# Kernel tuning notes

Hardware: AMD Instinct MI355X
Metric: run time of the kernel (lower is better)

Reference implementation:

```python
import jax, jax.numpy as jnp
import numpy as np

BATCH = 8192
N = 32
A_NUM = 5
EPS = 1e-10
ALPHA = jnp.array([0.01, 0.25, 0.5, 0.9, 0.99], dtype=jnp.float32)


def setup_inputs() -> dict:
    key = jax.random.key(0)
    ks = jax.random.split(key, 9)
    stdv = 1.0 / np.sqrt(N)
    u = lambda k, shape: jax.random.uniform(k, shape, jnp.float32, -stdv, stdv)
    L = N * (N - 1) // 2
    return {
        "inputs": jax.random.normal(ks[0], (BATCH, N, N), jnp.float32),
        "state": jax.random.normal(ks[1], (BATCH, A_NUM * N * N), jnp.float32),
        "WR_root": u(ks[2], (A_NUM,)),
        "Wt_root": u(ks[3], (1,)),
        "Wphi_root": u(ks[4], (1,)),
        "Ws_root": u(ks[5], (A_NUM,)),
        "Br": u(ks[6], (L, 1)),
        "Bt": u(ks[7], (L, 1)),
        "By": u(ks[8], (L, 1)),
    }


def _skew(Bvec, n):
    # Replicates the torch loop: row 0 is zeros; row k (k>=1) gets B[k-1 : 2k-1]
    # in its first k columns (overlapping slices of the flat parameter vector).
    b = Bvec.reshape(-1)
    r = jnp.arange(n)[:, None]
    c = jnp.arange(n)[None, :]
    idx = jnp.clip(r - 1 + c, 0, b.shape[0] - 1)  # B[k-1+j] for entry (k, j)
    L = jnp.where(c < r, b[idx], jnp.zeros((), b.dtype))
    return L - L.T


def _cayley(S, n):
    # MatrixExp in the source: (I - S)^{-1} (I + S)
    I = jnp.eye(n, dtype=S.dtype)
    return jnp.linalg.solve(I - S, I + S)


def _translate(A, Bvec, n):
    # M @ A @ M.T with M the Cayley 'exp' of the skew matrix built from Bvec.
    M = _cayley(_skew(Bvec, n), n)
    return jnp.einsum('ij,bjk,lk->bil', M, A, M)


def _nus(W_root, A, eps):
    # Weighted average over the a_num axis with weights W_root^2 / (sum + eps).
    W = W_root * W_root
    return jnp.einsum('a,banm->bnm', W / (W.sum() + eps), A)


def reference(inputs, state, WR_root, Wt_root, Wphi_root, Ws_root, Br, Bt, By):
    Mt_1 = state.reshape(-1, A_NUM, N, N)                 # [B, a, n, n]
    X = inputs.reshape(BATCH, N, N)                       # [B, n, n]

    Yt = _nus(WR_root, Mt_1, EPS)                         # [B, n, n]
    Rt = _translate(Yt, Br, N)

    at = (Wt_root[0] ** 2) / ((Wt_root ** 2 + Wphi_root ** 2).sum() + EPS)
    Tt = (1.0 - at) * X + at * Rt                         # Frechet mean FM
    Phit = _translate(Tt, Bt, N)

    # Per-j Frechet means, vectorized over the a_num axis.
    a = ALPHA[None, :, None, None]
    Mt = (1.0 - a) * Mt_1 + a * Phit[:, None, :, :]       # [B, a, n, n]

    St = _nus(Ws_root, Mt, EPS)
    Ot = _translate(St, By, N)                            # [B, n, n]

    return Ot, Mt.reshape(-1, A_NUM, N, N)
```

## Files before the change

### kernel.cpp

```cpp
#include <hip/hip_runtime.h>

#define NB 8192
#define OT_ELEMS (NB * 1024)
#define EPSF 1e-10f

typedef __attribute__((ext_vector_type(4))) float f32x4;
typedef __attribute__((ext_vector_type(8))) short s16x8;

#define SBAR() __builtin_amdgcn_sched_barrier(0)
#define LGK()  do { SBAR(); asm volatile("s_waitcnt lgkmcnt(0)"); SBAR(); } while (0)

#define MFMA_B16(A, B, C) __builtin_amdgcn_mfma_f32_16x16x32_bf16((A), (B), (C), 0, 0, 0)

__global__ void cayley_kernel(const float* __restrict__ Br,
                              const float* __restrict__ Bt,
                              const float* __restrict__ By,
                              float* __restrict__ M_out) {
  __shared__ float A[32][33];
  __shared__ float R[32][33];
  const float* B = (blockIdx.x == 0) ? Br : (blockIdx.x == 1) ? Bt : By;
  const int t = threadIdx.x;
  const int i = t >> 5, j = t & 31;
  float Lij = (j < i) ? B[i - 1 + j] : 0.0f;
  float Lji = (i < j) ? B[j - 1 + i] : 0.0f;
  float S = Lij - Lji;
  float eye = (i == j) ? 1.0f : 0.0f;
  A[i][j] = eye - S;
  R[i][j] = eye + S;
  __syncthreads();
  for (int p = 0; p < 32; ++p) {
    float f = A[i][p] / A[p][p];
    __syncthreads();
    if (i != p) {
      A[i][j] -= f * A[p][j];
      R[i][j] -= f * R[p][j];
    }
    __syncthreads();
  }
  M_out[blockIdx.x * 1024 + i * 32 + j] = R[i][j] / A[i][i];
}

__global__ void combine_kernel(float* __restrict__ ws) {
  __shared__ float sMR[1024], sMT[1024];
  const int t = threadIdx.x;
  sMR[t] = ws[t];
  sMT[t] = ws[1024 + t];
  __syncthreads();
  const int i = t >> 5, j = t & 31;
  float s = 0.f;
#pragma unroll
  for (int k = 0; k < 32; ++k)
    s = fmaf(sMT[i * 32 + k], sMR[k * 32 + j], s);
  ws[3072 + i * 32 + j] = s;
}

__device__ __forceinline__ void cvt_hilo8(const f32x4 f0, const f32x4 f1, s16x8& hi, s16x8& lo) {
  float f[8];
#pragma unroll
  for (int e = 0; e < 4; ++e) { f[e] = f0[e]; f[4 + e] = f1[e]; }
#pragma unroll
  for (int e = 0; e < 8; ++e) {
    unsigned u = __float_as_uint(f[e]);
    hi[e] = (short)(u >> 16);
    float ah = __uint_as_float(u & 0xffff0000u);
    lo[e] = (short)(__float_as_uint(f[e] - ah) >> 16);
  }
}

__device__ __forceinline__ void read_frag_lds(const float* sb, int off, s16x8& hi, s16x8& lo) {
  f32x4 f0 = *(const f32x4*)(sb + off);
  f32x4 f1 = *(const f32x4*)(sb + off + 4);
  cvt_hilo8(f0, f1, hi, lo);
}

__global__ __launch_bounds__(64) void spdsru_main(
    const float* __restrict__ X, const float* __restrict__ state,
    const float* __restrict__ WR, const float* __restrict__ Wt,
    const float* __restrict__ Wphi, const float* __restrict__ Ws,
    const float* __restrict__ Mg, float* __restrict__ out) {
  __shared__ __align__(16) float sb0[1152];
  __shared__ __align__(16) float sb1[1152];
  __shared__ __align__(16) float sb2[1152];
  __shared__ __align__(16) float sb3[1152];
  const int lane = threadIdx.x;
  const int l15 = lane & 15, l4 = lane >> 4;
  const int i0 = (lane >> 3) << 2, j0 = (lane & 7) << 2;
  const int bid = blockIdx.x;
  const int batch = (bid & 7) * (NB >> 3) + (bid >> 3);

  s16x8 Mh[3][2], Ml[3][2];
  {
    const int srcoff[3] = {1024, 3072, 2048};
#pragma unroll
    for (int q = 0; q < 3; ++q)
#pragma unroll
      for (int s = 0; s < 2; ++s) {
        const float* p = Mg + srcoff[q] + (16 * s + l15) * 32 + 8 * l4;
        cvt_hilo8(*(const f32x4*)p, *(const f32x4*)(p + 4), Mh[q][s], Ml[q][s]);
      }
  }

  const float alpha[5] = {0.01f, 0.25f, 0.5f, 0.9f, 0.99f};
  float wr[5], va[5];
  float cP = 0.f;
  {
    float sR = 0.f, sS = 0.f, wq[5];
#pragma unroll
    for (int a = 0; a < 5; ++a) { float v = WR[a]; wr[a] = v * v; sR += v * v; }
#pragma unroll
    for (int a = 0; a < 5; ++a) { float v = Ws[a]; wq[a] = v * v; sS += v * v; }
    const float invR = 1.0f / (sR + EPSF), invS = 1.0f / (sS + EPSF);
#pragma unroll
    for (int a = 0; a < 5; ++a) {
      wr[a] *= invR;
      float w = wq[a] * invS;
      va[a] = w * (1.0f - alpha[a]);
      cP += w * alpha[a];
    }
  }
  const float wt2 = Wt[0] * Wt[0], wp2 = Wphi[0] * Wphi[0];
  const float at = wt2 / (wt2 + wp2 + EPSF);
  const float omat = 1.0f - at;

  const float* xp = X + (size_t)batch * 1024;
  f32x4 x[4];
#pragma unroll
  for (int r = 0; r < 4; ++r)
    x[r] = __builtin_nontemporal_load((const f32x4*)(xp + (i0 + r) * 32 + j0));

  const float* stp = state + (size_t)batch * 5120;
  f32x4 U[4], V[4];
#pragma unroll
  for (int r = 0; r < 4; ++r) { U[r] = f32x4{0.f, 0.f, 0.f, 0.f}; V[r] = U[r]; }
#pragma unroll
  for (int a = 0; a < 5; ++a)
#pragma unroll
    for (int r = 0; r < 4; ++r) {
      const f32x4 v = *(const f32x4*)(stp + a * 1024 + (i0 + r) * 32 + j0);
      U[r] += wr[a] * v;
      V[r] += va[a] * v;
    }

#pragma unroll
  for (int c = 0; c < 4; ++c) {
    f32x4 cx = {x[0][c], x[1][c], x[2][c], x[3][c]};
    f32x4 cu = {U[0][c], U[1][c], U[2][c], U[3][c]};
    *(f32x4*)(sb0 + (j0 + c) * 36 + i0) = cx;
    *(f32x4*)(sb1 + (j0 + c) * 36 + i0) = cu;
  }
  LGK();

  s16x8 BXh[2], BXl[2], BUh[2], BUl[2];
#pragma unroll
  for (int s = 0; s < 2; ++s) {
    read_frag_lds(sb0, (16 * s + l15) * 36 + 8 * l4, BXh[s], BXl[s]);
    read_frag_lds(sb1, (16 * s + l15) * 36 + 8 * l4, BUh[s], BUl[s]);
  }
  {
    f32x4 gX[2][2], gU[2][2];
#pragma unroll
    for (int ms = 0; ms < 2; ++ms)
#pragma unroll
      for (int ns = 0; ns < 2; ++ns) {
        f32x4 a0 = {0.f, 0.f, 0.f, 0.f};
        a0 = MFMA_B16(Ml[0][ms], BXh[ns], a0);
        a0 = MFMA_B16(Mh[0][ms], BXl[ns], a0);
        a0 = MFMA_B16(Mh[0][ms], BXh[ns], a0);
        gX[ms][ns] = a0;
        f32x4 a1 = {0.f, 0.f, 0.f, 0.f};
        a1 = MFMA_B16(Ml[1][ms], BUh[ns], a1);
        a1 = MFMA_B16(Mh[1][ms], BUl[ns], a1);
        a1 = MFMA_B16(Mh[1][ms], BUh[ns], a1);
        gU[ms][ns] = a1;
      }
#pragma unroll
    for (int ms = 0; ms < 2; ++ms)
#pragma unroll
      for (int ns = 0; ns < 2; ++ns)
#pragma unroll
        for (int r = 0; r < 4; ++r) {
          sb2[(16 * ms + 4 * l4 + r) * 36 + 16 * ns + l15] = gX[ms][ns][r];
          sb3[(16 * ms + 4 * l4 + r) * 36 + 16 * ns + l15] = gU[ms][ns][r];
        }
  }
  LGK();

  {
    s16x8 AXh[2], AXl[2], AUh[2], AUl[2];
#pragma unroll
    for (int s = 0; s < 2; ++s) {
      read_frag_lds(sb2, (16 * s + l15) * 36 + 8 * l4, AXh[s], AXl[s]);
      read_frag_lds(sb3, (16 * s + l15) * 36 + 8 * l4, AUh[s], AUl[s]);
    }
    f32x4 ph[2][2];
#pragma unroll
    for (int ms = 0; ms < 2; ++ms)
#pragma unroll
      for (int ns = 0; ns < 2; ++ns) {
        f32x4 a0 = {0.f, 0.f, 0.f, 0.f};
        a0 = MFMA_B16(AXl[ms], Mh[0][ns], a0);
        a0 = MFMA_B16(AXh[ms], Ml[0][ns], a0);
        a0 = MFMA_B16(AXh[ms], Mh[0][ns], a0);
        f32x4 a1 = {0.f, 0.f, 0.f, 0.f};
        a1 = MFMA_B16(AUl[ms], Mh[1][ns], a1);
        a1 = MFMA_B16(AUh[ms], Ml[1][ns], a1);
        a1 = MFMA_B16(AUh[ms], Mh[1][ns], a1);
        ph[ms][ns] = omat * a0 + at * a1;
      }
#pragma unroll
    for (int ms = 0; ms < 2; ++ms)
#pragma unroll
      for (int ns = 0; ns < 2; ++ns)
#pragma unroll
        for (int r = 0; r < 4; ++r)
          sb0[(16 * ms + 4 * l4 + r) * 36 + 16 * ns + l15] = ph[ms][ns][r];
  }
  LGK();

  f32x4 ph4[4];
#pragma unroll
  for (int r = 0; r < 4; ++r)
    ph4[r] = *(const f32x4*)(sb0 + (i0 + r) * 36 + j0);
  f32x4 st4[4];
#pragma unroll
  for (int r = 0; r < 4; ++r) st4[r] = V[r] + cP * ph4[r];
#pragma unroll
  for (int c = 0; c < 4; ++c) {
    f32x4 cs = {st4[0][c], st4[1][c], st4[2][c], st4[3][c]};
    *(f32x4*)(sb1 + (j0 + c) * 36 + i0) = cs;
  }
  f32x4 raw2[20];
#pragma unroll
  for (int a = 0; a < 5; ++a)
#pragma unroll
    for (int r = 0; r < 4; ++r)
      raw2[a * 4 + r] = *(const f32x4*)(stp + a * 1024 + (i0 + r) * 32 + j0);
  LGK();

  {
    s16x8 BSh[2], BSl[2];
#pragma unroll
    for (int s = 0; s < 2; ++s)
      read_frag_lds(sb1, (16 * s + l15) * 36 + 8 * l4, BSh[s], BSl[s]);
    f32x4 gS[2][2];
#pragma unroll
    for (int ms = 0; ms < 2; ++ms)
#pragma unroll
      for (int ns = 0; ns < 2; ++ns) {
        f32x4 acc = {0.f, 0.f, 0.f, 0.f};
        acc = MFMA_B16(Ml[2][ms], BSh[ns], acc);
        acc = MFMA_B16(Mh[2][ms], BSl[ns], acc);
        acc = MFMA_B16(Mh[2][ms], BSh[ns], acc);
        gS[ms][ns] = acc;
      }
    float* outMt = out + OT_ELEMS + (size_t)batch * 5120;
#pragma unroll
    for (int a = 0; a < 5; ++a) {
      const float al = alpha[a], om = 1.0f - al;
#pragma unroll
      for (int r = 0; r < 4; ++r) {
        f32x4 w = om * raw2[a * 4 + r] + al * ph4[r];
        __builtin_nontemporal_store(w, (f32x4*)(outMt + a * 1024 + (i0 + r) * 32 + j0));
      }
    }
#pragma unroll
    for (int ms = 0; ms < 2; ++ms)
#pragma unroll
      for (int ns = 0; ns < 2; ++ns)
#pragma unroll
        for (int r = 0; r < 4; ++r)
          sb2[(16 * ms + 4 * l4 + r) * 36 + 16 * ns + l15] = gS[ms][ns][r];
  }
  LGK();

  {
    s16x8 ASh[2], ASl[2];
#pragma unroll
    for (int s = 0; s < 2; ++s)
      read_frag_lds(sb2, (16 * s + l15) * 36 + 8 * l4, ASh[s], ASl[s]);
    f32x4 o[2][2];
#pragma unroll
    for (int ms = 0; ms < 2; ++ms)
#pragma unroll
      for (int ns = 0; ns < 2; ++ns) {
        f32x4 acc = {0.f, 0.f, 0.f, 0.f};
        acc = MFMA_B16(ASl[ms], Mh[2][ns], acc);
        acc = MFMA_B16(ASh[ms], Ml[2][ns], acc);
        acc = MFMA_B16(ASh[ms], Mh[2][ns], acc);
        o[ms][ns] = acc;
      }
#pragma unroll
    for (int ms = 0; ms < 2; ++ms)
#pragma unroll
      for (int ns = 0; ns < 2; ++ns)
#pragma unroll
        for (int r = 0; r < 4; ++r)
          sb3[(16 * ms + 4 * l4 + r) * 36 + 16 * ns + l15] = o[ms][ns][r];
  }
  LGK();

  float* outOt = out + (size_t)batch * 1024;
#pragma unroll
  for (int r = 0; r < 4; ++r) {
    f32x4 ov = *(const f32x4*)(sb3 + (i0 + r) * 36 + j0);
    __builtin_nontemporal_store(ov, (f32x4*)(outOt + (i0 + r) * 32 + j0));
  }
}

extern "C" void kernel_launch(void* const* d_in, const int* in_sizes, int n_in,
                              void* d_out, int out_size, void* d_ws, size_t ws_size,
                              hipStream_t stream) {
  const float* X     = (const float*)d_in[0];
  const float* state = (const float*)d_in[1];
  const float* WR    = (const float*)d_in[2];
  const float* Wt    = (const float*)d_in[3];
  const float* Wphi  = (const float*)d_in[4];
  const float* Ws    = (const float*)d_in[5];
  const float* Br    = (const float*)d_in[6];
  const float* Bt    = (const float*)d_in[7];
  const float* By    = (const float*)d_in[8];
  float* m_ws = (float*)d_ws;
  float* outp = (float*)d_out;

  cayley_kernel<<<3, 1024, 0, stream>>>(Br, Bt, By, m_ws);
  combine_kernel<<<1, 1024, 0, stream>>>(m_ws);
  spdsru_main<<<NB, 64, 0, stream>>>(X, state, WR, Wt, Wphi, Ws, m_ws, outp);
}
```

Baseline: 89.18 us.

## Split S=V+cP*Phi left-product across stages and store Ot directly from MFMA

```diff
diff --git a/kernel.cpp b/kernel.cpp
--- a/kernel.cpp
+++ b/kernel.cpp
@@ -11,6 +11,13 @@
 #define LGK()  do { SBAR(); asm volatile("s_waitcnt lgkmcnt(0)"); SBAR(); } while (0)
 
 #define MFMA_B16(A, B, C) __builtin_amdgcn_mfma_f32_16x16x32_bf16((A), (B), (C), 0, 0, 0)
+
+#define PROD3(ACC, AH, AL, BH, BL)             \
+  do {                                         \
+    ACC = MFMA_B16((AL), (BH), ACC);           \
+    ACC = MFMA_B16((AH), (BL), ACC);           \
+    ACC = MFMA_B16((AH), (BH), ACC);           \
+  } while (0)
 
 __global__ void cayley_kernel(const float* __restrict__ Br,
                               const float* __restrict__ Bt,
@@ -82,6 +89,7 @@
   __shared__ __align__(16) float sb1[1152];
   __shared__ __align__(16) float sb2[1152];
   __shared__ __align__(16) float sb3[1152];
+  __shared__ __align__(16) float sb4[1152];
   const int lane = threadIdx.x;
   const int l15 = lane & 15, l4 = lane >> 4;
   const int i0 = (lane >> 3) << 2, j0 = (lane & 7) << 2;
@@ -145,33 +153,36 @@
   for (int c = 0; c < 4; ++c) {
     f32x4 cx = {x[0][c], x[1][c], x[2][c], x[3][c]};
     f32x4 cu = {U[0][c], U[1][c], U[2][c], U[3][c]};
+    f32x4 cv = {V[0][c], V[1][c], V[2][c], V[3][c]};
     *(f32x4*)(sb0 + (j0 + c) * 36 + i0) = cx;
     *(f32x4*)(sb1 + (j0 + c) * 36 + i0) = cu;
+    *(f32x4*)(sb2 + (j0 + c) * 36 + i0) = cv;
   }
   LGK();
 
-  s16x8 BXh[2], BXl[2], BUh[2], BUl[2];
-#pragma unroll
-  for (int s = 0; s < 2; ++s) {
-    read_frag_lds(sb0, (16 * s + l15) * 36 + 8 * l4, BXh[s], BXl[s]);
-    read_frag_lds(sb1, (16 * s + l15) * 36 + 8 * l4, BUh[s], BUl[s]);
-  }
-  {
+  f32x4 gV[2][2];
+  {
+    s16x8 BXh[2], BXl[2], BUh[2], BUl[2], BVh[2], BVl[2];
+#pragma unroll
+    for (int s = 0; s < 2; ++s) {
+      read_frag_lds(sb0, (16 * s + l15) * 36 + 8 * l4, BXh[s], BXl[s]);
+      read_frag_lds(sb1, (16 * s + l15) * 36 + 8 * l4, BUh[s], BUl[s]);
+      read_frag_lds(sb2, (16 * s + l15) * 36 + 8 * l4, BVh[s], BVl[s]);
+    }
     f32x4 gX[2][2], gU[2][2];
 #pragma unroll
     for (int ms = 0; ms < 2; ++ms)
 #pragma unroll
       for (int ns = 0; ns < 2; ++ns) {
         f32x4 a0 = {0.f, 0.f, 0.f, 0.f};
-        a0 = MFMA_B16(Ml[0][ms], BXh[ns], a0);
-        a0 = MFMA_B16(Mh[0][ms], BXl[ns], a0);
-        a0 = MFMA_B16(Mh[0][ms], BXh[ns], a0);
+        PROD3(a0, Mh[0][ms], Ml[0][ms], BXh[ns], BXl[ns]);
         gX[ms][ns] = a0;
         f32x4 a1 = {0.f, 0.f, 0.f, 0.f};
-        a1 = MFMA_B16(Ml[1][ms], BUh[ns], a1);
-        a1 = MFMA_B16(Mh[1][ms], BUl[ns], a1);
-        a1 = MFMA_B16(Mh[1][ms], BUh[ns], a1);
+        PROD3(a1, Mh[1][ms], Ml[1][ms], BUh[ns], BUl[ns]);
         gU[ms][ns] = a1;
+        f32x4 a2 = {0.f, 0.f, 0.f, 0.f};
+        PROD3(a2, Mh[2][ms], Ml[2][ms], BVh[ns], BVl[ns]);
+        gV[ms][ns] = a2;
       }
 #pragma unroll
     for (int ms = 0; ms < 2; ++ms)
@@ -179,8 +190,8 @@
       for (int ns = 0; ns < 2; ++ns)
 #pragma unroll
         for (int r = 0; r < 4; ++r) {
-          sb2[(16 * ms + 4 * l4 + r) * 36 + 16 * ns + l15] = gX[ms][ns][r];
-          sb3[(16 * ms + 4 * l4 + r) * 36 + 16 * ns + l15] = gU[ms][ns][r];
+          sb3[(16 * ms + 4 * l4 + r) * 36 + 16 * ns + l15] = gX[ms][ns][r];
+          sb4[(16 * ms + 4 * l4 + r) * 36 + 16 * ns + l15] = gU[ms][ns][r];
         }
   }
   LGK();
@@ -189,8 +200,8 @@
     s16x8 AXh[2], AXl[2], AUh[2], AUl[2];
 #pragma unroll
     for (int s = 0; s < 2; ++s) {
-      read_frag_lds(sb2, (16 * s + l15) * 36 + 8 * l4, AXh[s], AXl[s]);
-      read_frag_lds(sb3, (16 * s + l15) * 36 + 8 * l4, AUh[s], AUl[s]);
+      read_frag_lds(sb3, (16 * s + l15) * 36 + 8 * l4, AXh[s], AXl[s]);
+      read_frag_lds(sb4, (16 * s + l15) * 36 + 8 * l4, AUh[s], AUl[s]);
     }
     f32x4 ph[2][2];
 #pragma unroll
@@ -198,60 +209,70 @@
 #pragma unroll
       for (int ns = 0; ns < 2; ++ns) {
         f32x4 a0 = {0.f, 0.f, 0.f, 0.f};
-        a0 = MFMA_B16(AXl[ms], Mh[0][ns], a0);
-        a0 = MFMA_B16(AXh[ms], Ml[0][ns], a0);
-        a0 = MFMA_B16(AXh[ms], Mh[0][ns], a0);
+        PROD3(a0, AXh[ms], AXl[ms], Mh[0][ns], Ml[0][ns]);
         f32x4 a1 = {0.f, 0.f, 0.f, 0.f};
-        a1 = MFMA_B16(AUl[ms], Mh[1][ns], a1);
-        a1 = MFMA_B16(AUh[ms], Ml[1][ns], a1);
-        a1 = MFMA_B16(AUh[ms], Mh[1][ns], a1);
+        PROD3(a1, AUh[ms], AUl[ms], Mh[1][ns], Ml[1][ns]);
         ph[ms][ns] = omat * a0 + at * a1;
       }
 #pragma unroll
     for (int ms = 0; ms < 2; ++ms)
 #pragma unroll
       for (int ns = 0; ns < 2; ++ns)
-#pragma unroll
-        for (int r = 0; r < 4; ++r)
-          sb0[(16 * ms + 4 * l4 + r) * 36 + 16 * ns + l15] = ph[ms][ns][r];
+        *(f32x4*)(sb0 + (16 * ns + l15) * 36 + 16 * ms + 4 * l4) = ph[ms][ns];
   }
   LGK();
 
-  f32x4 ph4[4];
-#pragma unroll
-  for (int r = 0; r < 4; ++r)
-    ph4[r] = *(const f32x4*)(sb0 + (i0 + r) * 36 + j0);
-  f32x4 st4[4];
-#pragma unroll
-  for (int r = 0; r < 4; ++r) st4[r] = V[r] + cP * ph4[r];
-#pragma unroll
-  for (int c = 0; c < 4; ++c) {
-    f32x4 cs = {st4[0][c], st4[1][c], st4[2][c], st4[3][c]};
-    *(f32x4*)(sb1 + (j0 + c) * 36 + i0) = cs;
-  }
   f32x4 raw2[20];
 #pragma unroll
   for (int a = 0; a < 5; ++a)
 #pragma unroll
     for (int r = 0; r < 4; ++r)
       raw2[a * 4 + r] = *(const f32x4*)(stp + a * 1024 + (i0 + r) * 32 + j0);
+  f32x4 ph4[4];
+  {
+    s16x8 Bph_h[2], Bph_l[2];
+#pragma unroll
+    for (int s = 0; s < 2; ++s)
+      read_frag_lds(sb0, (16 * s + l15) * 36 + 8 * l4, Bph_h[s], Bph_l[s]);
+    f32x4 pc[4];
+#pragma unroll
+    for (int c = 0; c < 4; ++c)
+      pc[c] = *(const f32x4*)(sb0 + (j0 + c) * 36 + i0);
+#pragma unroll
+    for (int r = 0; r < 4; ++r)
+      ph4[r] = f32x4{pc[0][r], pc[1][r], pc[2][r], pc[3][r]};
+    f32x4 gS[2][2];
+#pragma unroll
+    for (int ms = 0; ms < 2; ++ms)
+#pragma unroll
+      for (int ns = 0; ns < 2; ++ns) {
+        f32x4 a2 = {0.f, 0.f, 0.f, 0.f};
+        PROD3(a2, Mh[2][ms], Ml[2][ms], Bph_h[ns], Bph_l[ns]);
+        gS[ms][ns] = gV[ms][ns] + cP * a2;
+      }
+#pragma unroll
+    for (int ms = 0; ms < 2; ++ms)
+#pragma unroll
+      for (int ns = 0; ns < 2; ++ns)
+#pragma unroll
+        for (int r = 0; r < 4; ++r)
+          sb1[(16 * ms + 4 * l4 + r) * 36 + 16 * ns + l15] = gS[ms][ns][r];
+  }
   LGK();
 
   {
-    s16x8 BSh[2], BSl[2];
+    s16x8 ASh[2], ASl[2];
 #pragma unroll
     for (int s = 0; s < 2; ++s)
-      read_frag_lds(sb1, (16 * s + l15) * 36 + 8 * l4, BSh[s], BSl[s]);
-    f32x4 gS[2][2];
+      read_frag_lds(sb1, (16 * s + l15) * 36 + 8 * l4, ASh[s], ASl[s]);
+    f32x4 o[2][2];
 #pragma unroll
     for (int ms = 0; ms < 2; ++ms)
 #pragma unroll
       for (int ns = 0; ns < 2; ++ns) {
         f32x4 acc = {0.f, 0.f, 0.f, 0.f};
-        acc = MFMA_B16(Ml[2][ms], BSh[ns], acc);
-        acc = MFMA_B16(Mh[2][ms], BSl[ns], acc);
-        acc = MFMA_B16(Mh[2][ms], BSh[ns], acc);
-        gS[ms][ns] = acc;
+        PROD3(acc, ASh[ms], ASl[ms], Mh[2][ns], Ml[2][ns]);
+        o[ms][ns] = acc;
       }
     float* outMt = out + OT_ELEMS + (size_t)batch * 5120;
 #pragma unroll
@@ -263,47 +284,15 @@
         __builtin_nontemporal_store(w, (f32x4*)(outMt + a * 1024 + (i0 + r) * 32 + j0));
       }
     }
+    float* outOt = out + (size_t)batch * 1024;
 #pragma unroll
     for (int ms = 0; ms < 2; ++ms)
 #pragma unroll
       for (int ns = 0; ns < 2; ++ns)
 #pragma unroll
         for (int r = 0; r < 4; ++r)
-          sb2[(16 * ms + 4 * l4 + r) * 36 + 16 * ns + l15] = gS[ms][ns][r];
-  }
-  LGK();
-
-  {
-    s16x8 ASh[2], ASl[2];
-#pragma unroll
-    for (int s = 0; s < 2; ++s)
-      read_frag_lds(sb2, (16 * s + l15) * 36 + 8 * l4, ASh[s], ASl[s]);
-    f32x4 o[2][2];
-#pragma unroll
-    for (int ms = 0; ms < 2; ++ms)
-#pragma unroll
-      for (int ns = 0; ns < 2; ++ns) {
-        f32x4 acc = {0.f, 0.f, 0.f, 0.f};
-        acc = MFMA_B16(ASl[ms], Mh[2][ns], acc);
-        acc = MFMA_B16(ASh[ms], Ml[2][ns], acc);
-        acc = MFMA_B16(ASh[ms], Mh[2][ns], acc);
-        o[ms][ns] = acc;
-      }
-#pragma unroll
-    for (int ms = 0; ms < 2; ++ms)
-#pragma unroll
-      for (int ns = 0; ns < 2; ++ns)
-#pragma unroll
-        for (int r = 0; r < 4; ++r)
-          sb3[(16 * ms + 4 * l4 + r) * 36 + 16 * ns + l15] = o[ms][ns][r];
-  }
-  LGK();
-
-  float* outOt = out + (size_t)batch * 1024;
-#pragma unroll
-  for (int r = 0; r < 4; ++r) {
-    f32x4 ov = *(const f32x4*)(sb3 + (i0 + r) * 36 + j0);
-    __builtin_nontemporal_store(ov, (f32x4*)(outOt + (i0 + r) * 32 + j0));
+          __builtin_nontemporal_store(o[ms][ns][r],
+              outOt + (16 * ms + 4 * l4 + r) * 32 + 16 * ns + l15);
   }
 }
 
```

After: 89.95 us. No clear change (+0.9%).
